# Performance work log

Measured on AMD Instinct MI355X. Metric: run time of the kernel, lower is better.

Reference implementation:

```python
import jax, jax.numpy as jnp
import numpy as np

B, S, D, H = 2, 2048, 1024, 16
DH = D // H  # head_dim = 64


def setup_inputs() -> dict:
    key = jax.random.key(0)
    ks = jax.random.split(key, 10)
    inp = {
        "query": jax.random.normal(ks[0], (B, S, D), jnp.float32),
        "key": jax.random.normal(ks[1], (B, S, D), jnp.float32),
        "value": jax.random.normal(ks[2], (B, S, D), jnp.float32),
        "mask": jnp.ones((B, S), jnp.int32),
        # per-head q/k/v projections stacked over the head axis [H, D, DH]
        "Wq": jax.random.normal(ks[3], (H, D, DH), jnp.float32) * 0.02,
        "bq": jnp.zeros((H, DH), jnp.float32),
        "Wk": jax.random.normal(ks[4], (H, D, DH), jnp.float32) * 0.02,
        "bk": jnp.zeros((H, DH), jnp.float32),
        "Wv": jax.random.normal(ks[5], (H, D, DH), jnp.float32) * 0.02,
        "bv": jnp.zeros((H, DH), jnp.float32),
        # output projection fc: Linear(D, D)
        "Wo": jax.random.normal(ks[6], (D, D), jnp.float32) * 0.02,
        "bo": jnp.zeros((D,), jnp.float32),
    }
    return inp


def reference(query, key, value, mask, Wq, bq, Wk, bk, Wv, bv, Wo, bo):
    scale = 1.0 / jnp.sqrt(jnp.asarray(DH, query.dtype))
    # batched per-head projections: [B,S,D] x [H,D,DH] -> [B,H,S,DH]
    q = jnp.einsum('bsd,hde->bhse', query, Wq) + bq[None, :, None, :]
    k = jnp.einsum('bsd,hde->bhse', key, Wk) + bk[None, :, None, :]
    v = jnp.einsum('bsd,hde->bhse', value, Wv) + bv[None, :, None, :]
    # scaled dot-product attention scores [B,H,Sq,Sk]
    scores = jnp.einsum('bhqe,bhke->bhqk', q, k) * scale
    scores = jnp.where(mask[:, None, None, :] == 0, jnp.asarray(-1e9, scores.dtype), scores)
    attn = jax.nn.softmax(scores, axis=-1)
    ctx = jnp.einsum('bhqk,bhke->bhqe', attn, v)          # [B,H,S,DH]
    ctx = ctx.transpose(0, 2, 1, 3).reshape(query.shape[0], -1, H * DH)  # concat heads
    return ctx @ Wo + bo
```

## Files before the change

### kernel.cpp

```cpp
#include <hip/hip_runtime.h>
#include <stdint.h>
#include <math.h>


typedef __attribute__((ext_vector_type(8))) short short8;
typedef __attribute__((ext_vector_type(4))) float floatx4;

#define LOG2E 1.44269504088896340736f

__device__ __forceinline__ unsigned short f32_bf16(float f) {
  union { float f; unsigned u; } c; c.f = f;
  return (unsigned short)((c.u + 0x7FFFu + ((c.u >> 16) & 1u)) >> 16);
}
__device__ __forceinline__ float bf16_f32(unsigned short u) {
  union { unsigned u; float f; } c; c.u = ((unsigned)u) << 16;
  return c.f;
}
__device__ __forceinline__ void gld16(const void* g, void* l) {
  __builtin_amdgcn_global_load_lds((const __attribute__((address_space(1))) void*)g,
                                   (__attribute__((address_space(3))) void*)l, 16, 0, 0);
}


__global__ __launch_bounds__(256) void cvt3_kernel(
    const float* __restrict__ a, const float* __restrict__ b, const float* __restrict__ c,
    unsigned short* __restrict__ oa, unsigned short* __restrict__ ob, unsigned short* __restrict__ oc,
    const int* __restrict__ mask, float* __restrict__ mb, int n4) {
  int i = blockIdx.x * 256 + threadIdx.x;
  if (blockIdx.y == 0 && blockIdx.x < 16) {
    int j = blockIdx.x * 256 + threadIdx.x;
    mb[j] = (mask[j] == 0) ? (-1.0e9f * LOG2E) : 0.0f;
  }
  if (i >= n4) return;
  const float* in; unsigned short* out;
  if (blockIdx.y == 0) { in = a; out = oa; }
  else if (blockIdx.y == 1) { in = b; out = ob; }
  else { in = c; out = oc; }
  float4 v = reinterpret_cast<const float4*>(in)[i];
  ushort4 o;
  o.x = f32_bf16(v.x); o.y = f32_bf16(v.y); o.z = f32_bf16(v.z); o.w = f32_bf16(v.w);
  reinterpret_cast<ushort4*>(out)[i] = o;
}

__global__ __launch_bounds__(256) void transpose_w_kernel(
    const float* __restrict__ w0, const float* __restrict__ w1, const float* __restrict__ w2,
    const float* __restrict__ wo,
    unsigned short* __restrict__ o0, unsigned short* __restrict__ o1, unsigned short* __restrict__ o2,
    unsigned short* __restrict__ oo) {
  __shared__ float t[32][33];
  const int tx = threadIdx.x & 31, ty = threadIdx.x >> 5;
  const int zb = blockIdx.z;
  const float* in; unsigned short* out; int R, C, z, r0, c0;
  if (zb < 48) {
    if (blockIdx.y >= 2) return;
    const int sel = zb >> 4; z = zb & 15;
    in = (sel == 0) ? w0 : (sel == 1) ? w1 : w2;
    out = (sel == 0) ? o0 : (sel == 1) ? o1 : o2;
    R = 1024; C = 64;
  } else {
    in = wo; out = oo; R = 1024; C = 1024; z = 0;
  }
  r0 = blockIdx.x * 32; c0 = blockIdx.y * 32;
  const float* inp = in + (size_t)z * R * C;
  #pragma unroll
  for (int j = 0; j < 4; ++j)
    t[ty + j * 8][tx] = inp[(size_t)(r0 + ty + j * 8) * C + c0 + tx];
  __syncthreads();
  #pragma unroll
  for (int j = 0; j < 4; ++j)
    out[((size_t)z * C + c0 + ty + j * 8) * R + r0 + tx] = f32_bf16(t[tx][ty + j * 8]);
}


__device__ __forceinline__ void gemm_core(
    const unsigned short* __restrict__ A, const unsigned short* __restrict__ Bt,
    int K, int blockM, int blockN,
    unsigned short* As, unsigned short* Bs, floatx4 acc[4][4]) {
  const int tid = threadIdx.x;
  const int w = tid >> 6;
  const int lane = tid & 63;
  const int quad = lane >> 4, l15 = lane & 15;
  const int wm = w & 1, wn = w >> 1;
  const int srow = lane >> 2;
  const int scol = (lane & 3) * 8;

  #pragma unroll
  for (int mi = 0; mi < 4; ++mi)
    #pragma unroll
    for (int ni = 0; ni < 4; ++ni)
      acc[mi][ni] = (floatx4){0.f, 0.f, 0.f, 0.f};

  const unsigned short* Arow = A + (size_t)blockM * K + (size_t)srow * K + scol;
  const unsigned short* Brow = Bt + (size_t)blockN * K + (size_t)srow * K + scol;

  auto stage = [&](int k0, int buf) {
    unsigned short* Asb = As + buf * (128 * 32);
    unsigned short* Bsb = Bs + buf * (128 * 32);
    #pragma unroll
    for (int i = 0; i < 2; ++i) {
      int row = w * 32 + i * 16;
      gld16(Arow + (size_t)row * K + k0, Asb + row * 32);
      gld16(Brow + (size_t)row * K + k0, Bsb + row * 32);
    }
  };

  const int iters = K >> 5;
  stage(0, 0);
  for (int it = 0; it < iters; ++it) {
    __syncthreads();
    if (it + 1 < iters) stage((it + 1) * 32, (it + 1) & 1);
    const unsigned short* Asb = As + (it & 1) * (128 * 32);
    const unsigned short* Bsb = Bs + (it & 1) * (128 * 32);
    short8 bf[4];
    #pragma unroll
    for (int ni = 0; ni < 4; ++ni)
      bf[ni] = *(const short8*)(Bsb + (wn * 64 + ni * 16 + l15) * 32 + quad * 8);
    #pragma unroll
    for (int mi = 0; mi < 4; ++mi) {
      short8 af = *(const short8*)(Asb + (wm * 64 + mi * 16 + l15) * 32 + quad * 8);
      #pragma unroll
      for (int ni = 0; ni < 4; ++ni)
        acc[mi][ni] = __builtin_amdgcn_mfma_f32_16x16x32_bf16(af, bf[ni], acc[mi][ni], 0, 0, 0);
    }
  }
}

__global__ __launch_bounds__(256) void gemm_proj_kernel(
    const unsigned short* __restrict__ qin, const unsigned short* __restrict__ kin,
    const unsigned short* __restrict__ vin,
    const unsigned short* __restrict__ WqT, const unsigned short* __restrict__ WkT,
    const unsigned short* __restrict__ WvT,
    const float* __restrict__ bq, const float* __restrict__ bk, const float* __restrict__ bv,
    unsigned short* __restrict__ Qp, unsigned short* __restrict__ Kp,
    unsigned short* __restrict__ Vt) {
  __shared__ unsigned short As[2][128 * 32];
  __shared__ unsigned short Bs[2][128 * 32];
  const int z = blockIdx.y, bx = blockIdx.x;
  const unsigned short *A, *Bt;
  const float* bias;
  int blockM, blockN;
  if (z < 2) {
    blockN = (bx & 7) * 128; blockM = (bx >> 3) * 128;
    A = z ? kin : qin; Bt = z ? WkT : WqT; bias = z ? bk : bq;
  } else {
    blockM = (bx & 7) * 128; blockN = (bx >> 3) * 128;
    A = WvT; Bt = vin; bias = bv;
  }
  floatx4 acc[4][4];
  gemm_core(A, Bt, 1024, blockM, blockN, As[0], Bs[0], acc);

  const int tid = threadIdx.x, w = tid >> 6, lane = tid & 63;
  const int quad = lane >> 4, l15 = lane & 15;
  const int wm = w & 1, wn = w >> 1;

  if (z < 2) {
    unsigned short* outp = z ? Kp : Qp;
    #pragma unroll
    for (int mi = 0; mi < 4; ++mi)
      #pragma unroll
      for (int ni = 0; ni < 4; ++ni) {
        const int n = blockN + wn * 64 + ni * 16 + l15;
        const int h = n >> 6, e = n & 63;
        const float bvv = bias[n];
        #pragma unroll
        for (int r = 0; r < 4; ++r) {
          const int m = blockM + wm * 64 + mi * 16 + quad * 4 + r;
          const int b = m >> 11, s = m & 2047;
          outp[(((size_t)b * 16 + h) * 2048 + s) * 64 + e] = f32_bf16(acc[mi][ni][r] + bvv);
        }
      }
  } else {
    #pragma unroll
    for (int mi = 0; mi < 4; ++mi) {
      float br[4];
      #pragma unroll
      for (int r = 0; r < 4; ++r)
        br[r] = bias[blockM + wm * 64 + mi * 16 + quad * 4 + r];
      #pragma unroll
      for (int ni = 0; ni < 4; ++ni) {
        const int n = blockN + wn * 64 + ni * 16 + l15;
        const int b = n >> 11, s = n & 2047;
        #pragma unroll
        for (int r = 0; r < 4; ++r) {
          const int m = blockM + wm * 64 + mi * 16 + quad * 4 + r;
          const int h = m >> 6, e = m & 63;
          Vt[(((size_t)b * 16 + h) * 64 + e) * 2048 + s] = f32_bf16(acc[mi][ni][r] + br[r]);
        }
      }
    }
  }
}

__global__ __launch_bounds__(256) void gemm_out_kernel(
    const unsigned short* __restrict__ A, const unsigned short* __restrict__ Bt,
    const float* __restrict__ bias, float* __restrict__ out, int K, int N) {
  __shared__ unsigned short As[2][128 * 32];
  __shared__ unsigned short Bs[2][64 * 32];
  const int tid = threadIdx.x;
  const int w = tid >> 6, lane = tid & 63;
  const int quad = lane >> 4, l15 = lane & 15;
  const int wm = w & 1, wn = w >> 1;
  const int srow = lane >> 2;
  const int scol = (lane & 3) * 8;
  const int blockN = blockIdx.x * 64, blockM = blockIdx.y * 128;

  floatx4 acc[4][2];
  #pragma unroll
  for (int mi = 0; mi < 4; ++mi)
    #pragma unroll
    for (int ni = 0; ni < 2; ++ni)
      acc[mi][ni] = (floatx4){0.f, 0.f, 0.f, 0.f};

  const unsigned short* Arow = A + (size_t)blockM * K + (size_t)srow * K + scol;
  const unsigned short* Brow = Bt + (size_t)blockN * K + (size_t)srow * K + scol;

  auto stage = [&](int k0, int buf) {
    #pragma unroll
    for (int i = 0; i < 2; ++i) {
      int row = w * 32 + i * 16;
      gld16(Arow + (size_t)row * K + k0, As[buf] + row * 32);
    }
    gld16(Brow + (size_t)(w * 16) * K + k0, Bs[buf] + (w * 16) * 32);
  };

  const int iters = K >> 5;
  stage(0, 0);
  for (int it = 0; it < iters; ++it) {
    __syncthreads();
    if (it + 1 < iters) stage((it + 1) * 32, (it + 1) & 1);
    const unsigned short* Asb = As[it & 1];
    const unsigned short* Bsb = Bs[it & 1];
    short8 bf[2];
    #pragma unroll
    for (int ni = 0; ni < 2; ++ni)
      bf[ni] = *(const short8*)(Bsb + (wn * 32 + ni * 16 + l15) * 32 + quad * 8);
    #pragma unroll
    for (int mi = 0; mi < 4; ++mi) {
      short8 af = *(const short8*)(Asb + (wm * 64 + mi * 16 + l15) * 32 + quad * 8);
      #pragma unroll
      for (int ni = 0; ni < 2; ++ni)
        acc[mi][ni] = __builtin_amdgcn_mfma_f32_16x16x32_bf16(af, bf[ni], acc[mi][ni], 0, 0, 0);
    }
  }

  #pragma unroll
  for (int mi = 0; mi < 4; ++mi)
    #pragma unroll
    for (int ni = 0; ni < 2; ++ni) {
      const int n = blockN + wn * 32 + ni * 16 + l15;
      const float bv = bias[n];
      #pragma unroll
      for (int r = 0; r < 4; ++r) {
        const int m = blockM + wm * 64 + mi * 16 + quad * 4 + r;
        out[(size_t)m * N + n] = acc[mi][ni][r] + bv;
      }
    }
}


__global__ __launch_bounds__(256) void attn_kernel(
    const unsigned short* __restrict__ Q, const unsigned short* __restrict__ Kg,
    const unsigned short* __restrict__ Vt, const float* __restrict__ maskAdd,
    unsigned short* __restrict__ ctx) {
  const int S = 2048;
  const int tid = threadIdx.x;
  const int w = tid >> 6, lane = tid & 63, quad = lane >> 4, l15 = lane & 15;
  const int qb = blockIdx.x, bh = blockIdx.y;
  const int b = bh >> 4, h = bh & 15;
  const int q0 = qb * 128;

  __shared__ unsigned short Ks[2][128 * 64];
  __shared__ unsigned short Vs[2][64 * 128];
  __shared__ unsigned short Ps[4][32 * 64];
  unsigned short* Pw = Ps[w];

  const unsigned short* Qb = Q + (size_t)bh * S * 64;
  const unsigned short* Kb = Kg + (size_t)bh * S * 64;
  const unsigned short* Vb = Vt + (size_t)bh * 64 * S;
  const float* mb = maskAdd + (size_t)b * S;

  const float qs = 0.125f * LOG2E;
  short8 qf[2][2];
  #pragma unroll
  for (int mi = 0; mi < 2; ++mi)
    #pragma unroll
    for (int kq = 0; kq < 2; ++kq) {
      short8 v = *(const short8*)(Qb + (size_t)(q0 + w * 32 + mi * 16 + l15) * 64 + kq * 32 + quad * 8);
      #pragma unroll
      for (int j = 0; j < 8; ++j)
        v[j] = (short)f32_bf16(bf16_f32((unsigned short)v[j]) * qs);
      qf[mi][kq] = v;
    }

  short8 onesf;
  #pragma unroll
  for (int j = 0; j < 8; ++j) onesf[j] = (short)0x3F80;

  floatx4 O[2][4], ls[2];
  #pragma unroll
  for (int mi = 0; mi < 2; ++mi) {
    #pragma unroll
    for (int ne = 0; ne < 4; ++ne) O[mi][ne] = (floatx4){0.f, 0.f, 0.f, 0.f};
    ls[mi] = (floatx4){0.f, 0.f, 0.f, 0.f};
  }

  auto stage_kv = [&](int t, int buf) {
    const int kv0 = t * 128;
    #pragma unroll
    for (int i = 0; i < 4; ++i) {
      int r0 = w * 32 + i * 8;
      int row = r0 + (lane >> 3);
      int cg = (lane & 7) ^ (row & 7);
      gld16(Kb + (size_t)(kv0 + row) * 64 + cg * 8, Ks[buf] + r0 * 64);
    }
    #pragma unroll
    for (int i = 0; i < 4; ++i) {
      int r0 = w * 16 + i * 4;
      int row = r0 + (lane >> 4);
      int p = lane & 15;
      int cg = (p & 8) | ((p & 7) ^ (row & 7));
      gld16(Vb + (size_t)row * S + kv0 + cg * 8, Vs[buf] + r0 * 128);
    }
  };

  stage_kv(0, 0);
  for (int t = 0; t < 16; ++t) {
    const int kv0 = t * 128;
    __syncthreads();
    float ma[8];
    #pragma unroll
    for (int ni = 0; ni < 8; ++ni) ma[ni] = mb[kv0 + ni * 16 + l15];
    if (t + 1 < 16) stage_kv(t + 1, (t + 1) & 1);
    const unsigned short* Ksb = Ks[t & 1];
    const unsigned short* Vsb = Vs[t & 1];

    #pragma unroll
    for (int ph = 0; ph < 2; ++ph) {
      floatx4 sc[2][4];
      #pragma unroll
      for (int ni = 0; ni < 4; ++ni) {
        const int key = (ph * 4 + ni) * 16 + l15;
        short8 kf0 = *(const short8*)(Ksb + key * 64 + ((quad) ^ (l15 & 7)) * 8);
        short8 kf1 = *(const short8*)(Ksb + key * 64 + ((4 + quad) ^ (l15 & 7)) * 8);
        #pragma unroll
        for (int mi = 0; mi < 2; ++mi) {
          floatx4 s = (floatx4){0.f, 0.f, 0.f, 0.f};
          s = __builtin_amdgcn_mfma_f32_16x16x32_bf16(qf[mi][0], kf0, s, 0, 0, 0);
          s = __builtin_amdgcn_mfma_f32_16x16x32_bf16(qf[mi][1], kf1, s, 0, 0, 0);
          sc[mi][ni] = s;
        }
      }
      #pragma unroll
      for (int mi = 0; mi < 2; ++mi)
        #pragma unroll
        for (int r = 0; r < 4; ++r) {
          const int row = mi * 16 + quad * 4 + r;
          const int g = (row + (row >> 3)) & 7;
          #pragma unroll
          for (int ni = 0; ni < 4; ++ni) {
            float p = __builtin_amdgcn_exp2f(sc[mi][ni][r] + ma[ph * 4 + ni]);
            union { float f; unsigned u; } c; c.f = p;
            const int ch = (ni * 2 + (l15 >> 3)) ^ g;
            Pw[row * 64 + (ch & 7) * 8 + (l15 & 7)] = (unsigned short)(c.u >> 16);
          }
        }
      #pragma unroll
      for (int kkl = 0; kkl < 2; ++kkl) {
        const int kk = ph * 2 + kkl;
        short8 pfr[2], vf[4];
        #pragma unroll
        for (int mi = 0; mi < 2; ++mi) {
          const int gp = (2 * mi + l15 + (l15 >> 3)) & 7;
          pfr[mi] = *(const short8*)(Pw + (mi * 16 + l15) * 64 + ((kkl * 4 + quad) ^ gp) * 8);
        }
        #pragma unroll
        for (int ne = 0; ne < 4; ++ne) {
          const int c = kk * 4 + quad;
          vf[ne] = *(const short8*)(Vsb + (ne * 16 + l15) * 128 + ((c & 8) | ((c & 7) ^ (l15 & 7))) * 8);
        }
        #pragma unroll
        for (int mi = 0; mi < 2; ++mi) {
          #pragma unroll
          for (int ne = 0; ne < 4; ++ne)
            O[mi][ne] = __builtin_amdgcn_mfma_f32_16x16x32_bf16(pfr[mi], vf[ne], O[mi][ne], 0, 0, 0);
          ls[mi] = __builtin_amdgcn_mfma_f32_16x16x32_bf16(pfr[mi], onesf, ls[mi], 0, 0, 0);
        }
      }
    }
  }

  #pragma unroll
  for (int mi = 0; mi < 2; ++mi)
    #pragma unroll
    for (int r = 0; r < 4; ++r) {
      const float inv = __builtin_amdgcn_rcpf(ls[mi][r]);
      const int s = q0 + w * 32 + mi * 16 + quad * 4 + r;
      #pragma unroll
      for (int ne = 0; ne < 4; ++ne)
        ctx[((size_t)b * S + s) * 1024 + h * 64 + ne * 16 + l15] = f32_bf16(O[mi][ne][r] * inv);
    }
}


extern "C" void kernel_launch(void* const* d_in, const int* in_sizes, int n_in,
                              void* d_out, int out_size, void* d_ws, size_t ws_size,
                              hipStream_t stream) {
  const float* query = (const float*)d_in[0];
  const float* key   = (const float*)d_in[1];
  const float* value = (const float*)d_in[2];
  const int*   mask  = (const int*)d_in[3];
  const float* Wq = (const float*)d_in[4];
  const float* bq = (const float*)d_in[5];
  const float* Wk = (const float*)d_in[6];
  const float* bk = (const float*)d_in[7];
  const float* Wv = (const float*)d_in[8];
  const float* bv = (const float*)d_in[9];
  const float* Wo = (const float*)d_in[10];
  const float* bo = (const float*)d_in[11];
  float* out = (float*)d_out;

  char* ws = (char*)d_ws;
  const size_t MB = 1024 * 1024;
  unsigned short* qin  = (unsigned short*)(ws + 0);
  unsigned short* kin  = (unsigned short*)(ws + 8 * MB);
  unsigned short* vin  = (unsigned short*)(ws + 16 * MB);
  unsigned short* WqT  = (unsigned short*)(ws + 24 * MB);
  unsigned short* WkT  = (unsigned short*)(ws + 26 * MB);
  unsigned short* WvT  = (unsigned short*)(ws + 28 * MB);
  unsigned short* WoT  = (unsigned short*)(ws + 30 * MB);
  unsigned short* Qp   = (unsigned short*)(ws + 32 * MB);
  unsigned short* Kp   = (unsigned short*)(ws + 40 * MB);
  unsigned short* Vt   = (unsigned short*)(ws + 48 * MB);
  float* maskAdd       = (float*)(ws + 56 * MB);
  unsigned short* ctxb = qin;

  cvt3_kernel<<<dim3(4096, 3), 256, 0, stream>>>(query, key, value, qin, kin, vin,
                                                 mask, maskAdd, 1048576);
  transpose_w_kernel<<<dim3(32, 32, 49), 256, 0, stream>>>(Wq, Wk, Wv, Wo, WqT, WkT, WvT, WoT);
  gemm_proj_kernel<<<dim3(256, 3), 256, 0, stream>>>(qin, kin, vin, WqT, WkT, WvT,
                                                     bq, bk, bv, Qp, Kp, Vt);
  attn_kernel<<<dim3(16, 32), 256, 0, stream>>>(Qp, Kp, Vt, maskAdd, ctxb);
  gemm_out_kernel<<<dim3(16, 32), 256, 0, stream>>>(ctxb, WoT, bo, out, 1024, 1024);
}
```

Before: 258.1 us.

## Merge prep kernels and remap block indices for XCD-aware L2 locality

Folds the bf16 conversion, mask bias and weight transpose kernels into one launch. The old transpose grid launched many blocks that returned immediately, and those are gone. It also remaps the block indices of the projection GEMM, attention and output GEMM so that blocks sharing an operand (same head or same A rows) land on the same XCD under round-robin dispatch, improving L2 reuse. Costs are index arithmetic and a possible change in tail balance.

```diff
diff --git a/kernel.cpp b/kernel.cpp
--- a/kernel.cpp
+++ b/kernel.cpp
@@ -22,45 +22,42 @@
 }
 
 
-__global__ __launch_bounds__(256) void cvt3_kernel(
-    const float* __restrict__ a, const float* __restrict__ b, const float* __restrict__ c,
-    unsigned short* __restrict__ oa, unsigned short* __restrict__ ob, unsigned short* __restrict__ oc,
-    const int* __restrict__ mask, float* __restrict__ mb, int n4) {
-  int i = blockIdx.x * 256 + threadIdx.x;
-  if (blockIdx.y == 0 && blockIdx.x < 16) {
-    int j = blockIdx.x * 256 + threadIdx.x;
-    mb[j] = (mask[j] == 0) ? (-1.0e9f * LOG2E) : 0.0f;
-  }
-  if (i >= n4) return;
-  const float* in; unsigned short* out;
-  if (blockIdx.y == 0) { in = a; out = oa; }
-  else if (blockIdx.y == 1) { in = b; out = ob; }
-  else { in = c; out = oc; }
-  float4 v = reinterpret_cast<const float4*>(in)[i];
-  ushort4 o;
-  o.x = f32_bf16(v.x); o.y = f32_bf16(v.y); o.z = f32_bf16(v.z); o.w = f32_bf16(v.w);
-  reinterpret_cast<ushort4*>(out)[i] = o;
-}
-
-__global__ __launch_bounds__(256) void transpose_w_kernel(
+__global__ __launch_bounds__(256) void prep_kernel(
+    const float* __restrict__ qf, const float* __restrict__ kf, const float* __restrict__ vf,
     const float* __restrict__ w0, const float* __restrict__ w1, const float* __restrict__ w2,
-    const float* __restrict__ wo,
+    const float* __restrict__ wo, const int* __restrict__ mask,
+    unsigned short* __restrict__ oq, unsigned short* __restrict__ ok, unsigned short* __restrict__ ov,
     unsigned short* __restrict__ o0, unsigned short* __restrict__ o1, unsigned short* __restrict__ o2,
-    unsigned short* __restrict__ oo) {
+    unsigned short* __restrict__ oo, float* __restrict__ mb) {
   __shared__ float t[32][33];
+  const int y = blockIdx.y, bx = blockIdx.x;
+  if (y < 3) {
+    if (y == 0 && bx < 16) {
+      int j = bx * 256 + threadIdx.x;
+      mb[j] = (mask[j] == 0) ? (-1.0e9f * LOG2E) : 0.0f;
+    }
+    const float* in = (y == 0) ? qf : (y == 1) ? kf : vf;
+    unsigned short* out = (y == 0) ? oq : (y == 1) ? ok : ov;
+    int i = bx * 256 + threadIdx.x;
+    float4 v = reinterpret_cast<const float4*>(in)[i];
+    ushort4 o;
+    o.x = f32_bf16(v.x); o.y = f32_bf16(v.y); o.z = f32_bf16(v.z); o.w = f32_bf16(v.w);
+    reinterpret_cast<ushort4*>(out)[i] = o;
+    return;
+  }
   const int tx = threadIdx.x & 31, ty = threadIdx.x >> 5;
-  const int zb = blockIdx.z;
   const float* in; unsigned short* out; int R, C, z, r0, c0;
-  if (zb < 48) {
-    if (blockIdx.y >= 2) return;
+  if (bx < 3072) {
+    const int zb = bx >> 6, rem = bx & 63;
     const int sel = zb >> 4; z = zb & 15;
     in = (sel == 0) ? w0 : (sel == 1) ? w1 : w2;
     out = (sel == 0) ? o0 : (sel == 1) ? o1 : o2;
-    R = 1024; C = 64;
+    R = 1024; C = 64; r0 = (rem >> 1) * 32; c0 = (rem & 1) * 32;
   } else {
+    const int t2 = bx - 3072;
     in = wo; out = oo; R = 1024; C = 1024; z = 0;
-  }
-  r0 = blockIdx.x * 32; c0 = blockIdx.y * 32;
+    r0 = (t2 >> 5) * 32; c0 = (t2 & 31) * 32;
+  }
   const float* inp = in + (size_t)z * R * C;
   #pragma unroll
   for (int j = 0; j < 4; ++j)
@@ -136,14 +133,17 @@
   __shared__ unsigned short As[2][128 * 32];
   __shared__ unsigned short Bs[2][128 * 32];
   const int z = blockIdx.y, bx = blockIdx.x;
+  const int r = bx & 7, j = bx >> 3;
   const unsigned short *A, *Bt;
   const float* bias;
   int blockM, blockN;
   if (z < 2) {
-    blockN = (bx & 7) * 128; blockM = (bx >> 3) * 128;
+    blockM = (r * 4 + (j & 3)) * 128;
+    blockN = (j >> 2) * 128;
     A = z ? kin : qin; Bt = z ? WkT : WqT; bias = z ? bk : bq;
   } else {
-    blockM = (bx & 7) * 128; blockN = (bx >> 3) * 128;
+    blockN = (r * 4 + (j & 3)) * 128;
+    blockM = (j >> 2) * 128;
     A = WvT; Bt = vin; bias = bv;
   }
   floatx4 acc[4][4];
@@ -163,10 +163,10 @@
         const int h = n >> 6, e = n & 63;
         const float bvv = bias[n];
         #pragma unroll
-        for (int r = 0; r < 4; ++r) {
-          const int m = blockM + wm * 64 + mi * 16 + quad * 4 + r;
+        for (int rr = 0; rr < 4; ++rr) {
+          const int m = blockM + wm * 64 + mi * 16 + quad * 4 + rr;
           const int b = m >> 11, s = m & 2047;
-          outp[(((size_t)b * 16 + h) * 2048 + s) * 64 + e] = f32_bf16(acc[mi][ni][r] + bvv);
+          outp[(((size_t)b * 16 + h) * 2048 + s) * 64 + e] = f32_bf16(acc[mi][ni][rr] + bvv);
         }
       }
   } else {
@@ -174,17 +174,17 @@
     for (int mi = 0; mi < 4; ++mi) {
       float br[4];
       #pragma unroll
-      for (int r = 0; r < 4; ++r)
-        br[r] = bias[blockM + wm * 64 + mi * 16 + quad * 4 + r];
+      for (int rr = 0; rr < 4; ++rr)
+        br[rr] = bias[blockM + wm * 64 + mi * 16 + quad * 4 + rr];
       #pragma unroll
       for (int ni = 0; ni < 4; ++ni) {
         const int n = blockN + wn * 64 + ni * 16 + l15;
         const int b = n >> 11, s = n & 2047;
         #pragma unroll
-        for (int r = 0; r < 4; ++r) {
-          const int m = blockM + wm * 64 + mi * 16 + quad * 4 + r;
+        for (int rr = 0; rr < 4; ++rr) {
+          const int m = blockM + wm * 64 + mi * 16 + quad * 4 + rr;
           const int h = m >> 6, e = m & 63;
-          Vt[(((size_t)b * 16 + h) * 64 + e) * 2048 + s] = f32_bf16(acc[mi][ni][r] + br[r]);
+          Vt[(((size_t)b * 16 + h) * 64 + e) * 2048 + s] = f32_bf16(acc[mi][ni][rr] + br[rr]);
         }
       }
     }
@@ -202,7 +202,9 @@
   const int wm = w & 1, wn = w >> 1;
   const int srow = lane >> 2;
   const int scol = (lane & 3) * 8;
-  const int blockN = blockIdx.x * 64, blockM = blockIdx.y * 128;
+  const int l = blockIdx.x, r = l & 7, j = l >> 3;
+  const int blockM = (r * 4 + (j & 3)) * 128;
+  const int blockN = (j >> 2) * 64;
 
   floatx4 acc[4][2];
   #pragma unroll
@@ -250,9 +252,9 @@
       const int n = blockN + wn * 32 + ni * 16 + l15;
       const float bv = bias[n];
       #pragma unroll
-      for (int r = 0; r < 4; ++r) {
-        const int m = blockM + wm * 64 + mi * 16 + quad * 4 + r;
-        out[(size_t)m * N + n] = acc[mi][ni][r] + bv;
+      for (int rr = 0; rr < 4; ++rr) {
+        const int m = blockM + wm * 64 + mi * 16 + quad * 4 + rr;
+        out[(size_t)m * N + n] = acc[mi][ni][rr] + bv;
       }
     }
 }
@@ -265,7 +267,9 @@
   const int S = 2048;
   const int tid = threadIdx.x;
   const int w = tid >> 6, lane = tid & 63, quad = lane >> 4, l15 = lane & 15;
-  const int qb = blockIdx.x, bh = blockIdx.y;
+  const int l = blockIdx.x, r8 = l & 7, j8 = l >> 3;
+  const int bh = r8 * 4 + (j8 & 3);
+  const int qb = j8 >> 2;
   const int b = bh >> 4, h = bh & 15;
   const int q0 = qb * 128;
 
@@ -287,14 +291,14 @@
     for (int kq = 0; kq < 2; ++kq) {
       short8 v = *(const short8*)(Qb + (size_t)(q0 + w * 32 + mi * 16 + l15) * 64 + kq * 32 + quad * 8);
       #pragma unroll
-      for (int j = 0; j < 8; ++j)
-        v[j] = (short)f32_bf16(bf16_f32((unsigned short)v[j]) * qs);
+      for (int jj = 0; jj < 8; ++jj)
+        v[jj] = (short)f32_bf16(bf16_f32((unsigned short)v[jj]) * qs);
       qf[mi][kq] = v;
     }
 
   short8 onesf;
   #pragma unroll
-  for (int j = 0; j < 8; ++j) onesf[j] = (short)0x3F80;
+  for (int jj = 0; jj < 8; ++jj) onesf[jj] = (short)0x3F80;
 
   floatx4 O[2][4], ls[2];
   #pragma unroll
@@ -353,12 +357,12 @@
       #pragma unroll
       for (int mi = 0; mi < 2; ++mi)
         #pragma unroll
-        for (int r = 0; r < 4; ++r) {
-          const int row = mi * 16 + quad * 4 + r;
+        for (int rr = 0; rr < 4; ++rr) {
+          const int row = mi * 16 + quad * 4 + rr;
           const int g = (row + (row >> 3)) & 7;
           #pragma unroll
           for (int ni = 0; ni < 4; ++ni) {
-            float p = __builtin_amdgcn_exp2f(sc[mi][ni][r] + ma[ph * 4 + ni]);
+            float p = __builtin_amdgcn_exp2f(sc[mi][ni][rr] + ma[ph * 4 + ni]);
             union { float f; unsigned u; } c; c.f = p;
             const int ch = (ni * 2 + (l15 >> 3)) ^ g;
             Pw[row * 64 + (ch & 7) * 8 + (l15 & 7)] = (unsigned short)(c.u >> 16);
@@ -367,7 +371,7 @@
       #pragma unroll
       for (int kkl = 0; kkl < 2; ++kkl) {
         const int kk = ph * 2 + kkl;
-        short8 pfr[2], vf[4];
+        short8 pfr[2], vfr[4];
         #pragma unroll
         for (int mi = 0; mi < 2; ++mi) {
           const int gp = (2 * mi + l15 + (l15 >> 3)) & 7;
@@ -376,13 +380,13 @@
         #pragma unroll
         for (int ne = 0; ne < 4; ++ne) {
           const int c = kk * 4 + quad;
-          vf[ne] = *(const short8*)(Vsb + (ne * 16 + l15) * 128 + ((c & 8) | ((c & 7) ^ (l15 & 7))) * 8);
+          vfr[ne] = *(const short8*)(Vsb + (ne * 16 + l15) * 128 + ((c & 8) | ((c & 7) ^ (l15 & 7))) * 8);
         }
         #pragma unroll
         for (int mi = 0; mi < 2; ++mi) {
           #pragma unroll
           for (int ne = 0; ne < 4; ++ne)
-            O[mi][ne] = __builtin_amdgcn_mfma_f32_16x16x32_bf16(pfr[mi], vf[ne], O[mi][ne], 0, 0, 0);
+            O[mi][ne] = __builtin_amdgcn_mfma_f32_16x16x32_bf16(pfr[mi], vfr[ne], O[mi][ne], 0, 0, 0);
           ls[mi] = __builtin_amdgcn_mfma_f32_16x16x32_bf16(pfr[mi], onesf, ls[mi], 0, 0, 0);
         }
       }
@@ -392,12 +396,12 @@
   #pragma unroll
   for (int mi = 0; mi < 2; ++mi)
     #pragma unroll
-    for (int r = 0; r < 4; ++r) {
-      const float inv = __builtin_amdgcn_rcpf(ls[mi][r]);
-      const int s = q0 + w * 32 + mi * 16 + quad * 4 + r;
+    for (int rr = 0; rr < 4; ++rr) {
+      const float inv = __builtin_amdgcn_rcpf(ls[mi][rr]);
+      const int s = q0 + w * 32 + mi * 16 + quad * 4 + rr;
       #pragma unroll
       for (int ne = 0; ne < 4; ++ne)
-        ctx[((size_t)b * S + s) * 1024 + h * 64 + ne * 16 + l15] = f32_bf16(O[mi][ne][r] * inv);
+        ctx[((size_t)b * S + s) * 1024 + h * 64 + ne * 16 + l15] = f32_bf16(O[mi][ne][rr] * inv);
     }
 }
 
@@ -434,11 +438,10 @@
   float* maskAdd       = (float*)(ws + 56 * MB);
   unsigned short* ctxb = qin;
 
-  cvt3_kernel<<<dim3(4096, 3), 256, 0, stream>>>(query, key, value, qin, kin, vin,
-                                                 mask, maskAdd, 1048576);
-  transpose_w_kernel<<<dim3(32, 32, 49), 256, 0, stream>>>(Wq, Wk, Wv, Wo, WqT, WkT, WvT, WoT);
+  prep_kernel<<<dim3(4096, 4), 256, 0, stream>>>(query, key, value, Wq, Wk, Wv, Wo, mask,
+                                                 qin, kin, vin, WqT, WkT, WvT, WoT, maskAdd);
   gemm_proj_kernel<<<dim3(256, 3), 256, 0, stream>>>(qin, kin, vin, WqT, WkT, WvT,
                                                      bq, bk, bv, Qp, Kp, Vt);
-  attn_kernel<<<dim3(16, 32), 256, 0, stream>>>(Qp, Kp, Vt, maskAdd, ctxb);
-  gemm_out_kernel<<<dim3(16, 32), 256, 0, stream>>>(ctxb, WoT, bo, out, 1024, 1024);
-}
+  attn_kernel<<<dim3(512), 256, 0, stream>>>(Qp, Kp, Vt, maskAdd, ctxb);
+  gemm_out_kernel<<<dim3(512), 256, 0, stream>>>(ctxb, WoT, bo, out, 1024, 1024);
+}
```

Result: faster. 242.1 us (-6.2%).
